# Kernel tuning notes

Measured on AMD Instinct MI355X. Metric: run time of the kernel, lower is better.

Reference implementation:

```python
import jax, jax.numpy as jnp
import numpy as np

T = 1 << 20          # sequence length
THRESHOLD = 1e-4     # decay-reset threshold (module default)


def setup_inputs() -> dict:
    key = jax.random.key(0)
    X = jax.random.normal(key, (T,), dtype=jnp.float32)
    # stable params near module init [0.2, 0.2, 0.0, 0.0]; small w3/w4 keep the
    # quadratic recurrence bounded while exercising all terms.
    params = jnp.array([0.2, 0.2, 0.05, 0.01], dtype=jnp.float32)
    return {"X": X, "params": params}


def reference(X, params):
    dt = X.dtype
    w1 = jnp.tanh(params[0]); dtanh1 = 1.0 - w1 * w1; d2tanh1 = -2.0 * w1 * dtanh1
    w2 = jnp.tanh(params[1]); dtanh2 = 1.0 - w2 * w2; d2tanh2 = -2.0 * w2 * dtanh2
    w3, w4 = params[2], params[3]

    def step(carry, x):
        h, Jh, Hh, decay = carry  # h:(), Jh:(4,), Hh:(4,4), decay:()
        h_new = w1 * x + w2 * h + w3 * x * x + w4 * h * h
        df_dw = jnp.stack([x * dtanh1, h * dtanh2, x * x, h * h])
        df_dh = w2 + 2.0 * w4 * h
        Jh_new = df_dw + df_dh * Jh
        Hww = (jnp.zeros((4, 4), dt)
               .at[0, 0].set(x * d2tanh1)
               .at[1, 1].set(h * d2tanh2))
        g = jnp.zeros((4,), dt).at[1].set(dtanh2).at[3].set(2.0 * h)
        outer = g[:, None] * Jh[None, :]
        Hh_new = Hww + outer + outer.T + df_dh * Hh
        decay_new = decay * jnp.abs(df_dh)
        reset = decay_new < THRESHOLD
        # torch zero_() mutates storage in-place, so the appended J/H entries at a
        # reset step are also zeroed -> emit post-reset values.
        Jh_out = jnp.where(reset, jnp.zeros((4,), dt), Jh_new)
        Hh_out = jnp.where(reset, jnp.zeros((4, 4), dt), Hh_new)
        h_out = jnp.where(reset, jax.lax.stop_gradient(h_new), h_new)  # detach
        decay_out = jnp.where(reset, jnp.ones((), dt), decay_new)
        return (h_out, Jh_out, Hh_out, decay_out), (h_new, Jh_out, Hh_out)

    init = (jnp.zeros((), dt), jnp.zeros((4,), dt), jnp.zeros((4, 4), dt),
            jnp.ones((), dt))
    _, (hs, Js, Hs) = jax.lax.scan(step, init, X[:-1])
    Z = jnp.concatenate([jnp.zeros((1,), dt), hs])              # [T]
    J = jnp.concatenate([jnp.zeros((1, 4), dt), Js])            # [T, 4]
    H = jnp.concatenate([jnp.zeros((1, 4, 4), dt), Hs])         # [T, 4, 4]
    return Z, J, H
```

## Files before the change

kernel.cpp:

```cpp
#include <hip/hip_runtime.h>
#include <math.h>

#define TLEN (1 << 20)
#define SB 32
#define NSB (TLEN / SB)
#define SCB 512
#define NSCB (NSB / SCB)
#define THRESH 1e-4f
#define IDMAP 0x00FAC688u

#define WWORDS (SCB * SB + 8)
#define WPAD(i) ((i) + ((i) >> 5))
#define LDSW WPAD(WWORDS)

#pragma clang fp contract(off)


#define CHUNK55(OFS, OUTARR) {                                                 \
        const float4* xp_ = (const float4*)(X + (OFS) - 24);                   \
        float xa_[56];                                                         \
        _Pragma("unroll")                                                      \
        for (int q_ = 0; q_ < 14; ++q_) {                                      \
            float4 v_ = xp_[q_];                                               \
            xa_[4 * q_ + 0] = v_.x; xa_[4 * q_ + 1] = v_.y;                    \
            xa_[4 * q_ + 2] = v_.z; xa_[4 * q_ + 3] = v_.w;                    \
        }                                                                      \
        float h_ = 0.0f;                                                       \
        _Pragma("unroll")                                                      \
        for (int p_ = 0; p_ < 55; ++p_) {                                      \
            float x_ = xa_[p_];                                                \
            float t1_ = w1 * x_;                                               \
            float t2_ = w2 * h_;                                               \
            float s1_ = t1_ + t2_;                                             \
            float t3_ = (w3 * x_) * x_;                                        \
            float s2_ = s1_ + t3_;                                             \
            float t4_ = (w4 * h_) * h_;                                        \
            h_ = s2_ + t4_;                                                    \
            if (p_ >= 23) OUTARR[p_ - 23] = h_;                                \
        }                                                                      \
    }

__global__ void __launch_bounds__(512) k_zts(const float* __restrict__ P,
                                             const float* __restrict__ X,
                                             float* __restrict__ c,
                                             float* __restrict__ Z,
                                             unsigned int* __restrict__ L32,
                                             unsigned int* __restrict__ BT) {
#pragma clang fp contract(off)
    __shared__ float sc[4];
    __shared__ float zw[LDSW];
    __shared__ unsigned int buf[2][SCB];
    int t = threadIdx.x;
    int b = blockIdx.x;
    if (t == 0) {
        float tw1 = (float)tanh((double)P[0]);
        float tw2 = (float)tanh((double)P[1]);
        sc[0] = tw1; sc[1] = tw2; sc[2] = P[2]; sc[3] = P[3];
        if (b == 0) {
            float dt1 = 1.0f - tw1 * tw1;
            float dt2 = 1.0f - tw2 * tw2;
            c[0] = tw1; c[1] = tw2; c[2] = P[2]; c[3] = P[3];
            c[4] = dt1; c[5] = dt2;
            c[6] = (-2.0f * tw1) * dt1; c[7] = (-2.0f * tw2) * dt2;
            c[8] = 2.0f * P[3];
        }
    }
    __syncthreads();
    float w1 = sc[0], w2 = sc[1], w3 = sc[2], w4 = sc[3];
    float w42 = 2.0f * w4;
    long gi = (long)b * SCB + t;
    long o = gi * 32;
    float out[32];
    if (gi == 0) {
        float h = 0.0f;
        out[0] = 0.0f;
        for (int k = 0; k < 31; ++k) {
            float x = X[k];
            float t1 = w1 * x;
            float t2 = w2 * h;
            float s1 = t1 + t2;
            float t3 = (w3 * x) * x;
            float s2 = s1 + t3;
            float t4 = (w4 * h) * h;
            h = s2 + t4;
            out[k + 1] = h;
        }
    } else {
        CHUNK55(o, out);
    }
#pragma unroll
    for (int q = 0; q < 8; ++q)
        *(float4*)(Z + o + 4 * q) = make_float4(out[4 * q], out[4 * q + 1],
                                                out[4 * q + 2], out[4 * q + 3]);
    int rbase = t * 32 + 8;
#pragma unroll
    for (int k = 0; k < 32; ++k) zw[WPAD(rbase + k)] = out[k];
    if (t == 0 && b > 0) {
        long op = (long)b * (SCB * SB) - 32;
        float pout[32];
        CHUNK55(op, pout);
#pragma unroll
        for (int q = 0; q < 7; ++q) zw[WPAD(1 + q)] = pout[25 + q];
    }
    __syncthreads();
    unsigned int m32;
    if (gi < NSB - 1) {
        float d[8]; int last[8];
#pragma unroll
        for (int g = 0; g < 8; ++g) { d[g] = 1.0f; last[g] = -g; }
        if (gi == 0) {
#pragma unroll
            for (int g = 0; g < 8; ++g) last[g] = 0;
            for (int k = 0; k < 32; ++k) {
                float fa = fabsf(w2 + w42 * zw[WPAD(rbase + k)]);
#pragma unroll
                for (int g = 0; g < 8; ++g) {
                    d[g] = d[g] * fa;
                    if (d[g] < THRESH) { last[g] = k + 1; d[g] = 1.0f; }
                }
            }
        } else {
#pragma unroll
            for (int p = 0; p < 7; ++p) {
                float fa = fabsf(w2 + w42 * zw[WPAD(rbase + p - 7)]);
#pragma unroll
                for (int g = 7 - p; g < 8; ++g) {
                    d[g] = d[g] * fa;
                    if (d[g] < THRESH) { last[g] = p - 6; d[g] = 1.0f; }
                }
            }
            for (int k = 0; k < 32; ++k) {
                float fa = fabsf(w2 + w42 * zw[WPAD(rbase + k)]);
#pragma unroll
                for (int g = 0; g < 8; ++g) {
                    d[g] = d[g] * fa;
                    if (d[g] < THRESH) { last[g] = k + 1; d[g] = 1.0f; }
                }
            }
        }
        m32 = 0;
#pragma unroll
        for (int g = 0; g < 8; ++g) {
            int delta = 32 - last[g]; if (delta > 7) delta = 7;
            m32 |= (unsigned int)delta << (3 * g);
        }
    } else {
        m32 = IDMAP;
    }
    buf[0][t] = m32;
    __syncthreads();
    int cur = 0;
    for (int off = 1; off < SCB; off <<= 1) {
        unsigned int hi = buf[cur][t];
        unsigned int r;
        if (t >= off) {
            unsigned int lo = buf[cur][t - off];
            r = 0;
#pragma unroll
            for (int g = 0; g < 8; ++g) {
                unsigned int lg = (lo >> (3 * g)) & 7u;
                r |= ((hi >> (3 * lg)) & 7u) << (3 * g);
            }
        } else {
            r = hi;
        }
        buf[cur ^ 1][t] = r;
        __syncthreads();
        cur ^= 1;
    }
    L32[gi] = buf[cur][t];
    if (t == SCB - 1) BT[b] = buf[cur][t];
}

__global__ void __launch_bounds__(256) k_jh4(const float* __restrict__ X,
                                             const float* __restrict__ Z,
                                             const float* __restrict__ c,
                                             const unsigned int* __restrict__ L32,
                                             const unsigned int* __restrict__ BT,
                                             float* __restrict__ Jout,
                                             float* __restrict__ Hout) {
#pragma clang fp contract(off)
    __shared__ unsigned int sBT[NSCB];
    __shared__ unsigned char ages[256];
    __shared__ float hx[256 * 17];
    int t = threadIdx.x;
    int B = blockIdx.x;
    float w2 = c[1], dt1 = c[4], dt2 = c[5], d2t1 = c[6], d2t2 = c[7], w42 = c[8];
    if (t < NSCB) sBT[t] = BT[t];
    __syncthreads();
    if (t < 8) {
        int i = B * 8 + t;
        int e = 0;
        if (i > 0) {
            int bp = (i - 1) >> 9;
            unsigned int g = 0;
            for (int k = 0; k < bp; ++k) g = (sBT[k] >> (3 * g)) & 7u;
            e = (int)((L32[i - 1] >> (3 * g)) & 7u);
        }
        long ci = (long)i * SB;
        long r = ci - e;
        float d = 1.0f;
        long last = r;
        for (long m = r + 1; m <= ci; ++m) {
            float a = w2 + w42 * Z[m - 1];
            d = d * fabsf(a);
            if (d < THRESH) { last = m; d = 1.0f; }
        }
        ages[t * 32] = (unsigned char)(ci - last);
        for (int k = 1; k < SB; ++k) {
            long m = ci + k;
            float a = w2 + w42 * Z[m - 1];
            d = d * fabsf(a);
            if (d < THRESH) { last = m; d = 1.0f; }
            ages[t * 32 + k] = (unsigned char)(m - last);
        }
    }
    __syncthreads();
    long q = (long)B * 256 + t;
    int a = (int)ages[t];
    float J0 = 0, J1 = 0, J2 = 0, J3 = 0;
    float H00 = 0, H01 = 0, H03 = 0, H11 = 0, H12 = 0, H13 = 0, H23 = 0, H33 = 0;
    if (a > 0) {
        long m0 = q - a + 1;
        {
            float x = X[m0 - 1];
            float h = Z[m0 - 1];
            H00 = x * d2t1; H11 = h * d2t2;
            J0 = x * dt1; J1 = h * dt2; J2 = x * x; J3 = h * h;
        }
        for (long m = m0 + 1; m <= q; ++m) {
            float x = X[m - 1];
            float h = Z[m - 1];
            float av = w2 + w42 * h;
            float g3 = 2.0f * h;
            float g1J0 = dt2 * J0, g1J1 = dt2 * J1, g1J2 = dt2 * J2, g1J3 = dt2 * J3;
            float g3J0 = g3 * J0, g3J1 = g3 * J1, g3J2 = g3 * J2, g3J3 = g3 * J3;
            float n00 = (x * d2t1) + av * H00;
            float n01 = g1J0 + av * H01;
            float n03 = g3J0 + av * H03;
            float n11 = (((h * d2t2) + g1J1) + g1J1) + av * H11;
            float n12 = g1J2 + av * H12;
            float n13 = (g1J3 + g3J1) + av * H13;
            float n23 = g3J2 + av * H23;
            float n33 = (g3J3 + g3J3) + av * H33;
            H00 = n00; H01 = n01; H03 = n03; H11 = n11;
            H12 = n12; H13 = n13; H23 = n23; H33 = n33;
            J0 = (x * dt1) + av * J0;
            J1 = (h * dt2) + av * J1;
            J2 = (x * x) + av * J2;
            J3 = (h * h) + av * J3;
        }
    }
    *((float4*)(Jout + 4 * q)) = make_float4(J0, J1, J2, J3);
    float* hr = hx + t * 17;
    hr[0]  = H00; hr[1]  = H01; hr[2]  = 0.0f; hr[3]  = H03;
    hr[4]  = H01; hr[5]  = H11; hr[6]  = H12;  hr[7]  = H13;
    hr[8]  = 0.0f; hr[9] = H12; hr[10] = 0.0f; hr[11] = H23;
    hr[12] = H03; hr[13] = H13; hr[14] = H23;  hr[15] = H33;
    __syncthreads();
    float4* Hp = (float4*)Hout + (long)B * 1024;
#pragma unroll
    for (int r = 0; r < 4; ++r) {
        int f = 256 * r + t;
        int o = f >> 2;
        int cc = (f & 3) * 4;
        const float* s = hx + o * 17 + cc;
        Hp[f] = make_float4(s[0], s[1], s[2], s[3]);
    }
}

extern "C" void kernel_launch(void* const* d_in, const int* in_sizes, int n_in,
                              void* d_out, int out_size, void* d_ws, size_t ws_size,
                              hipStream_t stream) {
    const float* X = (const float*)d_in[0];
    const float* P = (const float*)d_in[1];
    float* out = (float*)d_out;
    float* Z = out;
    float* Jout = out + (long)TLEN;
    float* Hout = out + 5l * TLEN;

    char* ws = (char*)d_ws;
    float* consts = (float*)ws;
    unsigned int* BT = (unsigned int*)(ws + 64);
    unsigned int* L32 = (unsigned int*)(ws + 512);

    hipLaunchKernelGGL(k_zts, dim3(NSCB), dim3(SCB), 0, stream,
                       P, X, consts, Z, L32, BT);
    hipLaunchKernelGGL(k_jh4, dim3(TLEN / 256), dim3(256), 0, stream,
                       X, Z, consts, L32, BT, Jout, Hout);
}
```

Baseline: 43.89 us.

## Stage Z and X windows in LDS for Jacobian/Hessian kernel; halve scan block size

The Jacobian/Hessian kernel now cooperatively loads a 264-element window of Z and X per block into shared memory with float4 loads. The age computation and the per-thread recurrence then read from LDS instead of issuing scattered global loads. Separately, the scan superblock size drops from 512 to 256, so the first kernel launches twice as many blocks. The block-table walk, the bit shift and the workspace offset are adjusted to match, at the cost of a longer serial composition loop over block transitions.

```diff
diff --git a/kernel.cpp b/kernel.cpp
--- a/kernel.cpp
+++ b/kernel.cpp
@@ -4,7 +4,7 @@
 #define TLEN (1 << 20)
 #define SB 32
 #define NSB (TLEN / SB)
-#define SCB 512
+#define SCB 256
 #define NSCB (NSB / SCB)
 #define THRESH 1e-4f
 #define IDMAP 0x00FAC688u
@@ -40,7 +40,7 @@
         }                                                                      \
     }
 
-__global__ void __launch_bounds__(512) k_zts(const float* __restrict__ P,
+__global__ void __launch_bounds__(256) k_zts(const float* __restrict__ P,
                                              const float* __restrict__ X,
                                              float* __restrict__ c,
                                              float* __restrict__ Z,
@@ -172,7 +172,7 @@
     if (t == SCB - 1) BT[b] = buf[cur][t];
 }
 
-__global__ void __launch_bounds__(256) k_jh4(const float* __restrict__ X,
+__global__ void __launch_bounds__(256) k_jh6(const float* __restrict__ X,
                                              const float* __restrict__ Z,
                                              const float* __restrict__ c,
                                              const unsigned int* __restrict__ L32,
@@ -182,17 +182,39 @@
 #pragma clang fp contract(off)
     __shared__ unsigned int sBT[NSCB];
     __shared__ unsigned char ages[256];
+    __shared__ float zs[264];
+    __shared__ float xs[264];
     __shared__ float hx[256 * 17];
     int t = threadIdx.x;
     int B = blockIdx.x;
     float w2 = c[1], dt1 = c[4], dt2 = c[5], d2t1 = c[6], d2t2 = c[7], w42 = c[8];
+    long base = (long)B * 256 - 8;
     if (t < NSCB) sBT[t] = BT[t];
+    if (t >= 128 && t < 194) {
+        int s = t - 128;
+        long zi = base + 4l * s;
+        float4 v = make_float4(0.f, 0.f, 0.f, 0.f);
+        if (zi >= 0) v = *(const float4*)(Z + zi);
+        zs[4 * s] = v.x; zs[4 * s + 1] = v.y; zs[4 * s + 2] = v.z; zs[4 * s + 3] = v.w;
+    } else if (t >= 194 && t < 260 - 0 && t < 256) {
+        int s = t - 194;
+        long zi = base + 4l * s;
+        float4 v = make_float4(0.f, 0.f, 0.f, 0.f);
+        if (zi >= 0) v = *(const float4*)(X + zi);
+        xs[4 * s] = v.x; xs[4 * s + 1] = v.y; xs[4 * s + 2] = v.z; xs[4 * s + 3] = v.w;
+    } else if (t >= 64 && t < 68) {
+        int s = t - 64 + 62;
+        long zi = base + 4l * s;
+        float4 v = make_float4(0.f, 0.f, 0.f, 0.f);
+        if (zi >= 0) v = *(const float4*)(X + zi);
+        xs[4 * s] = v.x; xs[4 * s + 1] = v.y; xs[4 * s + 2] = v.z; xs[4 * s + 3] = v.w;
+    }
     __syncthreads();
     if (t < 8) {
         int i = B * 8 + t;
         int e = 0;
         if (i > 0) {
-            int bp = (i - 1) >> 9;
+            int bp = (i - 1) >> 8;
             unsigned int g = 0;
             for (int k = 0; k < bp; ++k) g = (sBT[k] >> (3 * g)) & 7u;
             e = (int)((L32[i - 1] >> (3 * g)) & 7u);
@@ -202,14 +224,14 @@
         float d = 1.0f;
         long last = r;
         for (long m = r + 1; m <= ci; ++m) {
-            float a = w2 + w42 * Z[m - 1];
+            float a = w2 + w42 * zs[(int)(m - 1 - base)];
             d = d * fabsf(a);
             if (d < THRESH) { last = m; d = 1.0f; }
         }
         ages[t * 32] = (unsigned char)(ci - last);
         for (int k = 1; k < SB; ++k) {
             long m = ci + k;
-            float a = w2 + w42 * Z[m - 1];
+            float a = w2 + w42 * zs[(int)(m - 1 - base)];
             d = d * fabsf(a);
             if (d < THRESH) { last = m; d = 1.0f; }
             ages[t * 32 + k] = (unsigned char)(m - last);
@@ -223,14 +245,16 @@
     if (a > 0) {
         long m0 = q - a + 1;
         {
-            float x = X[m0 - 1];
-            float h = Z[m0 - 1];
+            int ix = (int)(m0 - 1 - base);
+            float x = xs[ix];
+            float h = zs[ix];
             H00 = x * d2t1; H11 = h * d2t2;
             J0 = x * dt1; J1 = h * dt2; J2 = x * x; J3 = h * h;
         }
         for (long m = m0 + 1; m <= q; ++m) {
-            float x = X[m - 1];
-            float h = Z[m - 1];
+            int ix = (int)(m - 1 - base);
+            float x = xs[ix];
+            float h = zs[ix];
             float av = w2 + w42 * h;
             float g3 = 2.0f * h;
             float g1J0 = dt2 * J0, g1J1 = dt2 * J1, g1J2 = dt2 * J2, g1J3 = dt2 * J3;
@@ -260,8 +284,8 @@
     __syncthreads();
     float4* Hp = (float4*)Hout + (long)B * 1024;
 #pragma unroll
-    for (int r = 0; r < 4; ++r) {
-        int f = 256 * r + t;
+    for (int rr = 0; rr < 4; ++rr) {
+        int f = 256 * rr + t;
         int o = f >> 2;
         int cc = (f & 3) * 4;
         const float* s = hx + o * 17 + cc;
@@ -282,10 +306,10 @@
     char* ws = (char*)d_ws;
     float* consts = (float*)ws;
     unsigned int* BT = (unsigned int*)(ws + 64);
-    unsigned int* L32 = (unsigned int*)(ws + 512);
+    unsigned int* L32 = (unsigned int*)(ws + 1024);
 
     hipLaunchKernelGGL(k_zts, dim3(NSCB), dim3(SCB), 0, stream,
                        P, X, consts, Z, L32, BT);
-    hipLaunchKernelGGL(k_jh4, dim3(TLEN / 256), dim3(256), 0, stream,
+    hipLaunchKernelGGL(k_jh6, dim3(TLEN / 256), dim3(256), 0, stream,
                        X, Z, consts, L32, BT, Jout, Hout);
 }
```

After: 40.88 us. 6.9% less time.
